# Optimization experiments

Hardware: AMD Instinct MI355X
Metric: run time of the kernel (lower is better)

Reference implementation:

```python
import jax, jax.numpy as jnp
import numpy as np
import math

EPS = 1e-5

def layernorm(x, w):
    mu = jnp.mean(x, axis=-1, keepdims=True)
    var = jnp.var(x, axis=-1, keepdims=True)
    return (x - mu) * jax.lax.rsqrt(var + EPS) * w

def setup_inputs() -> dict:
    key = jax.random.key(0)
    ks = jax.random.split(key, 6)
    B, T, C = 2, 2048, 768
    s = 0.02
    return {
        "x": jax.random.normal(ks[0], (B, T, C), jnp.float32),
        "w_ln1": jnp.ones((C,), jnp.float32),
        "w_attn": jax.random.normal(ks[1], (C, 3 * C), jnp.float32) * s,
        "w_attn_proj": jax.random.normal(ks[2], (C, C), jnp.float32) * s,
        "w_ln2": jnp.ones((C,), jnp.float32),
        "w_fc": jax.random.normal(ks[3], (C, 4 * C), jnp.float32) * s,
        "w_mlp_proj": jax.random.normal(ks[4], (4 * C, C), jnp.float32) * s,
    }

def _attention(x, w_attn, w_attn_proj, n_head):
    B, T, C = x.shape
    D = C // n_head
    qkv = x @ w_attn  # [B,T,3C]
    q, k, v = jnp.split(qkv, 3, axis=-1)
    # [B,H,T,D]
    q = q.reshape(B, T, n_head, D).transpose(0, 2, 1, 3)
    k = k.reshape(B, T, n_head, D).transpose(0, 2, 1, 3)
    v = v.reshape(B, T, n_head, D).transpose(0, 2, 1, 3)
    # squared L2 distance via ||q||^2 + ||k||^2 - 2 q.k (same math, no [B,H,T,T,D] tensor)
    q2 = jnp.sum(q * q, axis=-1)  # [B,H,T]
    k2 = jnp.sum(k * k, axis=-1)  # [B,H,T]
    qk = jnp.einsum('bhqd,bhkd->bhqk', q, k)
    sq_l2 = q2[..., :, None] + k2[..., None, :] - 2.0 * qk  # [B,H,T,T]
    scale = -1.0 / (2.0 * math.sqrt(D))
    scores = jnp.exp(sq_l2 * scale)
    causal = jnp.tril(jnp.ones((T, T), bool))
    scores = jnp.where(causal[None, None], scores, 0.0)
    y = jnp.einsum('bhqk,bhkd->bhqd', scores, v)
    y = y.transpose(0, 2, 1, 3).reshape(B, T, C)
    return y @ w_attn_proj

def reference(x, w_ln1, w_attn, w_attn_proj, w_ln2, w_fc, w_mlp_proj):
    n_head = 12
    x = x + _attention(layernorm(x, w_ln1), w_attn, w_attn_proj, n_head)
    h = layernorm(x, w_ln2)
    h = jax.nn.gelu(h @ w_fc, approximate=False) @ w_mlp_proj
    return x + h
```

## Files before the change

### kernel.cpp

```cpp
#include <hip/hip_runtime.h>

typedef unsigned short u16;
typedef unsigned int u32;
typedef short bf16x8 __attribute__((ext_vector_type(8)));
typedef float f32x4 __attribute__((ext_vector_type(4)));

#define AS1 __attribute__((address_space(1)))
#define AS3 __attribute__((address_space(3)))

__device__ __forceinline__ float bf2f(u16 u){ return __uint_as_float(((u32)u)<<16); }
__device__ __forceinline__ u16 f2bf(float f){
  u32 x = __float_as_uint(f);
  x += 0x7fffu + ((x>>16)&1u);
  return (u16)(x>>16);
}
__device__ __forceinline__ float gelu_exact(float x){
  return 0.5f*x*(1.f + erff(x*0.7071067811865475f));
}

__global__ __launch_bounds__(256) void transpose_cast(
    const float* __restrict__ w, u16* __restrict__ wt, int K, int N)
{
  __shared__ float t[32][33];
  int lx = threadIdx.x & 31, ly = threadIdx.x >> 5;
  int n0 = blockIdx.x*32, k0 = blockIdx.y*32;
  #pragma unroll
  for (int j=0;j<4;j++) t[ly+j*8][lx] = w[(long)(k0+ly+j*8)*N + n0+lx];
  __syncthreads();
  #pragma unroll
  for (int j=0;j<4;j++) wt[(long)(n0+ly+j*8)*K + k0+lx] = f2bf(t[lx][ly+j*8]);
}

__global__ __launch_bounds__(256) void ln_rows(
    const float* __restrict__ x, const float* __restrict__ w, u16* __restrict__ out)
{
  int row = blockIdx.x, tid = threadIdx.x;
  const float* xr = x + (long)row*768;
  float v0 = xr[tid], v1 = xr[tid+256], v2 = xr[tid+512];
  float s = v0+v1+v2, sq = v0*v0+v1*v1+v2*v2;
  #pragma unroll
  for (int o=32;o>=1;o>>=1){ s += __shfl_down(s,o); sq += __shfl_down(sq,o); }
  __shared__ float red[8];
  int wv = tid>>6, ln = tid&63;
  if (ln==0){ red[wv]=s; red[wv+4]=sq; }
  __syncthreads();
  float S  = red[0]+red[1]+red[2]+red[3];
  float SQ = red[4]+red[5]+red[6]+red[7];
  float mu = S*(1.f/768.f);
  float var = SQ*(1.f/768.f) - mu*mu;
  float rstd = rsqrtf(var + 1e-5f);
  u16* o = out + (long)row*768;
  o[tid]     = f2bf((v0-mu)*rstd*w[tid]);
  o[tid+256] = f2bf((v1-mu)*rstd*w[tid+256]);
  o[tid+512] = f2bf((v2-mu)*rstd*w[tid+512]);
}

__global__ __launch_bounds__(256) void v_transpose(
    const u16* __restrict__ qkv, u16* __restrict__ vt)
{
  __shared__ __align__(16) u16 t[64*72];
  int b = blockIdx.z, h = blockIdx.y, t0 = blockIdx.x*64;
  int tid = threadIdx.x;
  int r = tid>>2, g = tid&3, c8 = g*16;
  const u16* src = qkv + ((long)(b*2048 + t0 + r))*2304 + 1536 + h*64 + c8;
  int wcol = c8 ^ (((r>>4)&3)*16);
  *(uint4*)&t[r*72 + wcol]     = *(const uint4*)src;
  *(uint4*)&t[r*72 + wcol + 8] = *(const uint4*)(src + 8);
  __syncthreads();
  int d = r;
  int rcol = d ^ (g*16);
  u32 pk[8];
  #pragma unroll
  for (int j=0;j<8;j++){
    u32 lo = t[(c8+2*j  )*72 + rcol];
    u32 hi = t[(c8+2*j+1)*72 + rcol];
    pk[j] = lo | (hi<<16);
  }
  u16* dst = vt + ((long)((b*12+h)*64 + d))*2048 + t0 + c8;
  uint4 o0 = {pk[0],pk[1],pk[2],pk[3]};
  uint4 o1 = {pk[4],pk[5],pk[6],pk[7]};
  *(uint4*)dst       = o0;
  *(uint4*)(dst + 8) = o1;
}

template<int EPI>
__global__ __launch_bounds__(256) void gemm_bt(
    const u16* __restrict__ A, const u16* __restrict__ BT,
    int M, int N, int K,
    u16* __restrict__ outB,
    float* __restrict__ q2g, float* __restrict__ k2g)
{
  __shared__ __align__(16) u16 As[2][128*32];
  __shared__ __align__(16) u16 Bs[2][128*32];
  int tid = threadIdx.x;
  int gx = gridDim.x;
  int nwg = gx * gridDim.y;
  int flat = blockIdx.x + gx*blockIdx.y;
  int cpx = nwg >> 3;
  int swz = (flat & 7)*cpx + (flat >> 3);
  int n0 = (swz % gx)*128, m0 = (swz / gx)*128;
  int w = tid>>6, lane = tid&63, lr = lane&15, lg = lane>>4;
  int wr = w>>1, wc = w&1;
  f32x4 acc[4][4];
  f32x4 z = {0.f,0.f,0.f,0.f};
  #pragma unroll
  for (int m=0;m<4;m++)
    #pragma unroll
    for (int n=0;n<4;n++) acc[m][n] = z;
  int rr16 = lane>>2, cc = (lane&3)*8;
  const u16* gA0 = A  + (long)(m0 + (2*w  )*16 + rr16)*K + cc;
  const u16* gA1 = A  + (long)(m0 + (2*w+1)*16 + rr16)*K + cc;
  const u16* gB0 = BT + (long)(n0 + (2*w  )*16 + rr16)*K + cc;
  const u16* gB1 = BT + (long)(n0 + (2*w+1)*16 + rr16)*K + cc;
  int o0 = (2*w)*512, o1 = (2*w+1)*512;
  __builtin_amdgcn_global_load_lds((const AS1 void*)gA0, (AS3 void*)(&As[0][o0]), 16, 0, 0);
  __builtin_amdgcn_global_load_lds((const AS1 void*)gA1, (AS3 void*)(&As[0][o1]), 16, 0, 0);
  __builtin_amdgcn_global_load_lds((const AS1 void*)gB0, (AS3 void*)(&Bs[0][o0]), 16, 0, 0);
  __builtin_amdgcn_global_load_lds((const AS1 void*)gB1, (AS3 void*)(&Bs[0][o1]), 16, 0, 0);
  gA0 += 32; gA1 += 32; gB0 += 32; gB1 += 32;
  __syncthreads();
  int cur = 0;
  for (int k0=0; k0<K; k0+=32){
    if (k0+32 < K){
      int nx = cur^1;
      __builtin_amdgcn_global_load_lds((const AS1 void*)gA0, (AS3 void*)(&As[nx][o0]), 16, 0, 0);
      __builtin_amdgcn_global_load_lds((const AS1 void*)gA1, (AS3 void*)(&As[nx][o1]), 16, 0, 0);
      __builtin_amdgcn_global_load_lds((const AS1 void*)gB0, (AS3 void*)(&Bs[nx][o0]), 16, 0, 0);
      __builtin_amdgcn_global_load_lds((const AS1 void*)gB1, (AS3 void*)(&Bs[nx][o1]), 16, 0, 0);
      gA0 += 32; gA1 += 32; gB0 += 32; gB1 += 32;
    }
    const u16* Ac = As[cur];
    const u16* Bc = Bs[cur];
    bf16x8 af[4], bfr[4];
    #pragma unroll
    for (int m=0;m<4;m++) af[m]  = *(const bf16x8*)&Ac[(wr*64+m*16+lr)*32 + lg*8];
    #pragma unroll
    for (int n=0;n<4;n++) bfr[n] = *(const bf16x8*)&Bc[(wc*64+n*16+lr)*32 + lg*8];
    #pragma unroll
    for (int m=0;m<4;m++)
      #pragma unroll
      for (int n=0;n<4;n++)
        acc[m][n] = __builtin_amdgcn_mfma_f32_16x16x32_bf16(af[m], bfr[n], acc[m][n], 0,0,0);
    __syncthreads();
    cur ^= 1;
  }
  if (EPI==0){
    #pragma unroll
    for (int m=0;m<4;m++){
      float s2[4] = {0.f,0.f,0.f,0.f};
      #pragma unroll
      for (int n=0;n<4;n++)
        #pragma unroll
        for (int r=0;r<4;r++){
          int row = m0 + wr*64 + m*16 + lg*4 + r;
          int col = n0 + wc*64 + n*16 + lr;
          u16 ub = f2bf(acc[m][n][r]);
          outB[(long)row*N + col] = ub;
          float vr = bf2f(ub);
          s2[r] += vr*vr;
        }
      #pragma unroll
      for (int r=0;r<4;r++){
        float t = s2[r];
        t += __shfl_xor(t,1); t += __shfl_xor(t,2); t += __shfl_xor(t,4); t += __shfl_xor(t,8);
        if (lr==0){
          int head = (n0 + wc*64) >> 6;
          int row = m0 + wr*64 + m*16 + lg*4 + r;
          int bb = row >> 11, tt = row & 2047;
          if (head < 12)      q2g[((long)(bb*12 + head     ))*2048 + tt] = t;
          else if (head < 24) k2g[((long)(bb*12 + head - 12))*2048 + tt] = t;
        }
      }
    }
  } else {
    #pragma unroll
    for (int m=0;m<4;m++)
      #pragma unroll
      for (int n=0;n<4;n++)
        #pragma unroll
        for (int r=0;r<4;r++){
          int row = m0 + wr*64 + m*16 + lg*4 + r;
          int col = n0 + wc*64 + n*16 + lr;
          outB[(long)row*N + col] = f2bf(gelu_exact(acc[m][n][r]));
        }
  }
}

__global__ __launch_bounds__(256) void gemm_ks(
    const u16* __restrict__ A, const u16* __restrict__ BT,
    int M, int N, int K, int KS,
    float* __restrict__ pb)
{
  __shared__ __align__(16) u16 As[2][128*32];
  __shared__ __align__(16) u16 Bs[2][64*32];
  int tid = threadIdx.x;
  int n0 = blockIdx.x*64, m0 = blockIdx.y*128;
  int kbeg = blockIdx.z*KS;
  int w = tid>>6, lane = tid&63, lr = lane&15, lg = lane>>4;
  int wr = w>>1, wc = w&1;
  f32x4 acc[4][2];
  f32x4 z = {0.f,0.f,0.f,0.f};
  #pragma unroll
  for (int m=0;m<4;m++){ acc[m][0]=z; acc[m][1]=z; }
  int rr16 = lane>>2, cc = (lane&3)*8;
  const u16* gA0 = A  + (long)(m0 + (2*w  )*16 + rr16)*K + kbeg + cc;
  const u16* gA1 = A  + (long)(m0 + (2*w+1)*16 + rr16)*K + kbeg + cc;
  const u16* gB0 = BT + (long)(n0 + w*16 + rr16)*K + kbeg + cc;
  int oa0 = (2*w)*512, oa1 = (2*w+1)*512, ob = w*512;
  __builtin_amdgcn_global_load_lds((const AS1 void*)gA0, (AS3 void*)(&As[0][oa0]), 16, 0, 0);
  __builtin_amdgcn_global_load_lds((const AS1 void*)gA1, (AS3 void*)(&As[0][oa1]), 16, 0, 0);
  __builtin_amdgcn_global_load_lds((const AS1 void*)gB0, (AS3 void*)(&Bs[0][ob ]), 16, 0, 0);
  gA0 += 32; gA1 += 32; gB0 += 32;
  __syncthreads();
  int cur = 0;
  for (int k0=0; k0<KS; k0+=32){
    if (k0+32 < KS){
      int nx = cur^1;
      __builtin_amdgcn_global_load_lds((const AS1 void*)gA0, (AS3 void*)(&As[nx][oa0]), 16, 0, 0);
      __builtin_amdgcn_global_load_lds((const AS1 void*)gA1, (AS3 void*)(&As[nx][oa1]), 16, 0, 0);
      __builtin_amdgcn_global_load_lds((const AS1 void*)gB0, (AS3 void*)(&Bs[nx][ob ]), 16, 0, 0);
      gA0 += 32; gA1 += 32; gB0 += 32;
    }
    const u16* Ac = As[cur];
    const u16* Bc = Bs[cur];
    bf16x8 af[4], bfr[2];
    #pragma unroll
    for (int m=0;m<4;m++) af[m]  = *(const bf16x8*)&Ac[(wr*64+m*16+lr)*32 + lg*8];
    #pragma unroll
    for (int n=0;n<2;n++) bfr[n] = *(const bf16x8*)&Bc[(wc*32+n*16+lr)*32 + lg*8];
    #pragma unroll
    for (int m=0;m<4;m++)
      #pragma unroll
      for (int n=0;n<2;n++)
        acc[m][n] = __builtin_amdgcn_mfma_f32_16x16x32_bf16(af[m], bfr[n], acc[m][n], 0,0,0);
    __syncthreads();
    cur ^= 1;
  }
  long zofs = (long)blockIdx.z*M*N;
  #pragma unroll
  for (int m=0;m<4;m++)
    #pragma unroll
    for (int n=0;n<2;n++)
      #pragma unroll
      for (int r=0;r<4;r++){
        int row = m0 + wr*64 + m*16 + lg*4 + r;
        int col = n0 + wc*32 + n*16 + lr;
        pb[zofs + (long)row*N + col] = acc[m][n][r];
      }
}

__global__ __launch_bounds__(256) void reduce2(
    const float* __restrict__ p, const float* __restrict__ resid,
    float* __restrict__ out, long n)
{
  long i = ((long)blockIdx.x*256 + threadIdx.x)*4;
  f32x4 a = *(const f32x4*)(resid+i);
  f32x4 b = *(const f32x4*)(p+i);
  f32x4 c = *(const f32x4*)(p+n+i);
  *(f32x4*)(out+i) = a+b+c;
}

__global__ __launch_bounds__(128) void attn_fused(
    const u16* __restrict__ qkv, const u16* __restrict__ vt,
    const float* __restrict__ q2g, const float* __restrict__ k2g,
    u16* __restrict__ Y)
{
  constexpr int C3=2304, C=768, T=2048, PADP=72;
  __shared__ __align__(16) u16 Ks[2][4096];
  __shared__ __align__(16) u16 Vs[2][4096];
  __shared__ __align__(16) u16 Ps[2][16*PADP];
  int bz = blockIdx.x;
  int swzb = (bz&7)*96 + (bz>>3);
  int sp = swzb & 31;
  int hh = (swzb>>5) % 12;
  int b  = swzb / 384;
  int tid = threadIdx.x, w = tid>>6, lane = tid&63, lr = lane&15, lg = lane>>4;
  long base = (long)b*T;
  long bh = (long)(b*12 + hh);
  const u16* kbase = qkv + base*C3 + C + hh*64;
  const u16* vbase = vt + bh*64*(long)T;
  const float* k2p = k2g + bh*T;
  const float* q2p0 = q2g + bh*T;

  int rowl = lane>>3;
  int c16 = (lane&7) ^ rowl;
  const u16* kp[4]; const u16* vp[4];
  #pragma unroll
  for (int i=0;i<4;i++){
    int c = w*4 + i;
    kp[i] = kbase + (long)(c*8 + rowl)*C3 + c16*8;
    vp[i] = vbase + (long)(c*8 + rowl)*T + c16*8;
  }
  u16* Pw = &Ps[w][0];
  f32x4 z = {0.f,0.f,0.f,0.f};

  for (int ph=0; ph<2; ++ph){
    int s = ph ? 63 - sp : sp;
    int ktl = s>>1;
    int qg0 = s*32 + w*16;
    const u16* qrow = qkv + (base + qg0 + lr)*C3 + hh*64;
    bf16x8 aq0 = *(const bf16x8*)(qrow + lg*8);
    bf16x8 aq1 = *(const bf16x8*)(qrow + 32 + lg*8);
    float q2m[4]; int qg[4];
    #pragma unroll
    for (int rr=0;rr<4;rr++){
      qg[rr] = qg0 + lg*4 + rr;
      q2m[rr] = 0.0625f * q2p0[qg[rr]];
    }
    f32x4 accY[4];
    #pragma unroll
    for (int i=0;i<4;i++) accY[i] = z;

    #pragma unroll
    for (int i=0;i<4;i++){
      __builtin_amdgcn_global_load_lds((const AS1 void*)kp[i], (AS3 void*)&Ks[0][(w*4+i)*512], 16, 0, 0);
      __builtin_amdgcn_global_load_lds((const AS1 void*)vp[i], (AS3 void*)&Vs[0][(w*4+i)*512], 16, 0, 0);
    }
    float k2n[4];
    #pragma unroll
    for (int nf=0;nf<4;nf++) k2n[nf] = k2p[nf*16+lr];
    __syncthreads();

    int cur = 0;
    for (int kt=0; kt<=ktl; ++kt){
      float k2c[4];
      #pragma unroll
      for (int i=0;i<4;i++) k2c[i] = k2n[i];
      if (kt < ktl){
        long kadd = (long)(kt+1)*64*C3;
        long vadd = (long)(kt+1)*64;
        #pragma unroll
        for (int i=0;i<4;i++){
          __builtin_amdgcn_global_load_lds((const AS1 void*)(kp[i]+kadd), (AS3 void*)&Ks[cur^1][(w*4+i)*512], 16, 0, 0);
          __builtin_amdgcn_global_load_lds((const AS1 void*)(vp[i]+vadd), (AS3 void*)&Vs[cur^1][(w*4+i)*512], 16, 0, 0);
        }
        #pragma unroll
        for (int nf=0;nf<4;nf++) k2n[nf] = k2p[(kt+1)*64 + nf*16+lr];
      }
      const u16* Kc = &Ks[cur][0];
      const u16* Vc = &Vs[cur][0];
      int kg0 = kt*64;
      #pragma unroll
      for (int nf=0;nf<4;nf++){
        int row = nf*16 + lr;
        int sw0 = ((lg    ) ^ (row&7))*8;
        int sw1 = ((4 | lg) ^ (row&7))*8;
        f32x4 sc = z;
        sc = __builtin_amdgcn_mfma_f32_16x16x32_bf16(aq0, *(const bf16x8*)&Kc[row*64 + sw0], sc, 0,0,0);
        sc = __builtin_amdgcn_mfma_f32_16x16x32_bf16(aq1, *(const bf16x8*)&Kc[row*64 + sw1], sc, 0,0,0);
        int kg = kg0 + row;
        float k2m = 0.0625f * k2c[nf];
        #pragma unroll
        for (int rr=0;rr<4;rr++){
          float e = __expf(0.125f*sc[rr] - q2m[rr] - k2m);
          e = (kg <= qg[rr]) ? e : 0.f;
          Pw[(lg*4+rr)*PADP + row] = f2bf(e);
        }
      }
      __builtin_amdgcn_wave_barrier();
      asm volatile("s_waitcnt lgkmcnt(0)" ::: "memory");
      bf16x8 ap0 = *(const bf16x8*)&Pw[lr*PADP + lg*8];
      bf16x8 ap1 = *(const bf16x8*)&Pw[lr*PADP + 32 + lg*8];
      #pragma unroll
      for (int nf=0;nf<4;nf++){
        int row = nf*16 + lr;
        int sw0 = ((lg    ) ^ (row&7))*8;
        int sw1 = ((4 | lg) ^ (row&7))*8;
        accY[nf] = __builtin_amdgcn_mfma_f32_16x16x32_bf16(ap0, *(const bf16x8*)&Vc[row*64 + sw0], accY[nf], 0,0,0);
        accY[nf] = __builtin_amdgcn_mfma_f32_16x16x32_bf16(ap1, *(const bf16x8*)&Vc[row*64 + sw1], accY[nf], 0,0,0);
      }
      __syncthreads();
      cur ^= 1;
    }
    #pragma unroll
    for (int nf=0;nf<4;nf++)
      #pragma unroll
      for (int rr=0;rr<4;rr++)
        Y[(base + qg0 + lg*4 + rr)*C + hh*64 + nf*16 + lr] = f2bf(accY[nf][rr]);
  }
}

extern "C" void kernel_launch(void* const* d_in, const int* in_sizes, int n_in,
                              void* d_out, int out_size, void* d_ws, size_t ws_size,
                              hipStream_t stream)
{
  (void)in_sizes; (void)n_in; (void)out_size; (void)ws_size;
  const float* x      = (const float*)d_in[0];
  const float* w_ln1  = (const float*)d_in[1];
  const float* w_attn = (const float*)d_in[2];
  const float* w_ap   = (const float*)d_in[3];
  const float* w_ln2  = (const float*)d_in[4];
  const float* w_fc   = (const float*)d_in[5];
  const float* w_mlp  = (const float*)d_in[6];
  float* out = (float*)d_out;
  const int M = 4096, T = 2048;
  const long NROW = (long)M*768;

  u16* ws      = (u16*)d_ws;
  u16* wT_attn = ws;
  u16* wT_ap   = wT_attn + 2304*768;
  u16* wT_fc   = wT_ap   + 768*768;
  u16* wT_mlp  = wT_fc   + 3072*768;
  u16* xln     = wT_mlp  + 768*3072;
  u16* qkvb    = xln     + 4096*768;
  u16* Ybuf    = qkvb    + 4096*2304;
  u16* hbuf    = qkvb;
  float* x2    = (float*)(Ybuf + 4096*768);
  u16* vtb     = (u16*)(x2 + 4096*768);
  float* q2g   = (float*)(vtb + 2*12*64*2048);
  float* k2g   = q2g + 24*2048;
  float* pbuf  = k2g + 24*2048;

  dim3 blk(256);
  transpose_cast<<<dim3(2304/32,  768/32), blk, 0, stream>>>(w_attn, wT_attn,  768, 2304);
  transpose_cast<<<dim3( 768/32,  768/32), blk, 0, stream>>>(w_ap,   wT_ap,    768,  768);
  transpose_cast<<<dim3(3072/32,  768/32), blk, 0, stream>>>(w_fc,   wT_fc,    768, 3072);
  transpose_cast<<<dim3( 768/32, 3072/32), blk, 0, stream>>>(w_mlp,  wT_mlp,  3072,  768);

  ln_rows<<<dim3(M), blk, 0, stream>>>(x, w_ln1, xln);
  gemm_bt<0><<<dim3(2304/128, M/128), blk, 0, stream>>>(xln, wT_attn, M, 2304, 768, qkvb, q2g, k2g);
  v_transpose<<<dim3(T/64, 12, 2), blk, 0, stream>>>(qkvb, vtb);
  attn_fused<<<dim3(2*12*32), dim3(128), 0, stream>>>(qkvb, vtb, q2g, k2g, Ybuf);
  gemm_ks<<<dim3(768/64, M/128, 2), blk, 0, stream>>>(Ybuf, wT_ap, M, 768, 768, 384, pbuf);
  reduce2<<<dim3(NROW/1024), blk, 0, stream>>>(pbuf, x, x2, NROW);
  ln_rows<<<dim3(M), blk, 0, stream>>>(x2, w_ln2, xln);
  gemm_bt<1><<<dim3(3072/128, M/128), blk, 0, stream>>>(xln, wT_fc, M, 3072, 768, hbuf, nullptr, nullptr);
  gemm_ks<<<dim3(768/64, M/128, 2), blk, 0, stream>>>(hbuf, wT_mlp, M, 768, 3072, 1536, pbuf);
  reduce2<<<dim3(NROW/1024), blk, 0, stream>>>(pbuf, x2, out, NROW);
}
```

Measured before the change: 297.0 us.

## Fuse residual reduce with LayerNorm, single-barrier GEMM pipelines, exp2 attention softmax

Replaces the separate reduce2 and ln_rows launches with one reduce2_ln kernel that sums the split-K partials and the residual, then normalizes the row. This saves a launch and a round trip through x2. Both GEMM kernels now use one barrier per k-step with explicit vmcnt waits, so the next tile's loads overlap the MFMAs. The attention kernel swaps the MFMA operands so each lane owns one query row, folds the scale constants into exp2, loads k2 as vectors, and packs the P stores into 64-bit writes. The hand-written waitcnt counts depend on the exact number of outstanding loads, so they are fragile.

```diff
diff --git a/kernel.cpp b/kernel.cpp
--- a/kernel.cpp
+++ b/kernel.cpp
@@ -7,6 +7,12 @@
 
 #define AS1 __attribute__((address_space(1)))
 #define AS3 __attribute__((address_space(3)))
+
+#if __has_builtin(__builtin_amdgcn_exp2f)
+#define EX2(x) __builtin_amdgcn_exp2f(x)
+#else
+#define EX2(x) exp2f(x)
+#endif
 
 __device__ __forceinline__ float bf2f(u16 u){ return __uint_as_float(((u32)u)<<16); }
 __device__ __forceinline__ u16 f2bf(float f){
@@ -55,6 +61,36 @@
   o[tid+512] = f2bf((v2-mu)*rstd*w[tid+512]);
 }
 
+__global__ __launch_bounds__(256) void reduce2_ln(
+    const float* __restrict__ p, const float* __restrict__ resid,
+    const float* __restrict__ w, float* __restrict__ x2, u16* __restrict__ xln, long n)
+{
+  int row = blockIdx.x, tid = threadIdx.x;
+  long off = (long)row*768;
+  float v[3];
+  #pragma unroll
+  for (int j=0;j<3;j++){
+    long i = off + tid + j*256;
+    v[j] = resid[i] + p[i] + p[n+i];
+    x2[i] = v[j];
+  }
+  float s = v[0]+v[1]+v[2], sq = v[0]*v[0]+v[1]*v[1]+v[2]*v[2];
+  #pragma unroll
+  for (int o=32;o>=1;o>>=1){ s += __shfl_down(s,o); sq += __shfl_down(sq,o); }
+  __shared__ float red[8];
+  int wv = tid>>6, ln = tid&63;
+  if (ln==0){ red[wv]=s; red[wv+4]=sq; }
+  __syncthreads();
+  float S  = red[0]+red[1]+red[2]+red[3];
+  float SQ = red[4]+red[5]+red[6]+red[7];
+  float mu = S*(1.f/768.f);
+  float var = SQ*(1.f/768.f) - mu*mu;
+  float rstd = rsqrtf(var + 1e-5f);
+  #pragma unroll
+  for (int j=0;j<3;j++)
+    xln[off + tid + j*256] = f2bf((v[j]-mu)*rstd*w[tid + j*256]);
+}
+
 __global__ __launch_bounds__(256) void v_transpose(
     const u16* __restrict__ qkv, u16* __restrict__ vt)
 {
@@ -118,9 +154,9 @@
   __builtin_amdgcn_global_load_lds((const AS1 void*)gB0, (AS3 void*)(&Bs[0][o0]), 16, 0, 0);
   __builtin_amdgcn_global_load_lds((const AS1 void*)gB1, (AS3 void*)(&Bs[0][o1]), 16, 0, 0);
   gA0 += 32; gA1 += 32; gB0 += 32; gB1 += 32;
-  __syncthreads();
   int cur = 0;
   for (int k0=0; k0<K; k0+=32){
+    __builtin_amdgcn_s_barrier();
     if (k0+32 < K){
       int nx = cur^1;
       __builtin_amdgcn_global_load_lds((const AS1 void*)gA0, (AS3 void*)(&As[nx][o0]), 16, 0, 0);
@@ -128,7 +164,11 @@
       __builtin_amdgcn_global_load_lds((const AS1 void*)gB0, (AS3 void*)(&Bs[nx][o0]), 16, 0, 0);
       __builtin_amdgcn_global_load_lds((const AS1 void*)gB1, (AS3 void*)(&Bs[nx][o1]), 16, 0, 0);
       gA0 += 32; gA1 += 32; gB0 += 32; gB1 += 32;
-    }
+      asm volatile("s_waitcnt vmcnt(4)" ::: "memory");
+    } else {
+      asm volatile("s_waitcnt vmcnt(0)" ::: "memory");
+    }
+    __builtin_amdgcn_sched_barrier(0);
     const u16* Ac = As[cur];
     const u16* Bc = Bs[cur];
     bf16x8 af[4], bfr[4];
@@ -141,7 +181,6 @@
       #pragma unroll
       for (int n=0;n<4;n++)
         acc[m][n] = __builtin_amdgcn_mfma_f32_16x16x32_bf16(af[m], bfr[n], acc[m][n], 0,0,0);
-    __syncthreads();
     cur ^= 1;
   }
   if (EPI==0){
@@ -211,16 +250,20 @@
   __builtin_amdgcn_global_load_lds((const AS1 void*)gA1, (AS3 void*)(&As[0][oa1]), 16, 0, 0);
   __builtin_amdgcn_global_load_lds((const AS1 void*)gB0, (AS3 void*)(&Bs[0][ob ]), 16, 0, 0);
   gA0 += 32; gA1 += 32; gB0 += 32;
-  __syncthreads();
   int cur = 0;
   for (int k0=0; k0<KS; k0+=32){
+    __builtin_amdgcn_s_barrier();
     if (k0+32 < KS){
       int nx = cur^1;
       __builtin_amdgcn_global_load_lds((const AS1 void*)gA0, (AS3 void*)(&As[nx][oa0]), 16, 0, 0);
       __builtin_amdgcn_global_load_lds((const AS1 void*)gA1, (AS3 void*)(&As[nx][oa1]), 16, 0, 0);
       __builtin_amdgcn_global_load_lds((const AS1 void*)gB0, (AS3 void*)(&Bs[nx][ob ]), 16, 0, 0);
       gA0 += 32; gA1 += 32; gB0 += 32;
-    }
+      asm volatile("s_waitcnt vmcnt(3)" ::: "memory");
+    } else {
+      asm volatile("s_waitcnt vmcnt(0)" ::: "memory");
+    }
+    __builtin_amdgcn_sched_barrier(0);
     const u16* Ac = As[cur];
     const u16* Bc = Bs[cur];
     bf16x8 af[4], bfr[2];
@@ -233,7 +276,6 @@
       #pragma unroll
       for (int n=0;n<2;n++)
         acc[m][n] = __builtin_amdgcn_mfma_f32_16x16x32_bf16(af[m], bfr[n], acc[m][n], 0,0,0);
-    __syncthreads();
     cur ^= 1;
   }
   long zofs = (long)blockIdx.z*M*N;
@@ -266,6 +308,8 @@
     u16* __restrict__ Y)
 {
   constexpr int C3=2304, C=768, T=2048, PADP=72;
+  constexpr float C1 = 0.18033688f;
+  constexpr float S2 = 0.09016844f;
   __shared__ __align__(16) u16 Ks[2][4096];
   __shared__ __align__(16) u16 Vs[2][4096];
   __shared__ __align__(16) u16 Ps[2][16*PADP];
@@ -301,12 +345,8 @@
     const u16* qrow = qkv + (base + qg0 + lr)*C3 + hh*64;
     bf16x8 aq0 = *(const bf16x8*)(qrow + lg*8);
     bf16x8 aq1 = *(const bf16x8*)(qrow + 32 + lg*8);
-    float q2m[4]; int qg[4];
-    #pragma unroll
-    for (int rr=0;rr<4;rr++){
-      qg[rr] = qg0 + lg*4 + rr;
-      q2m[rr] = 0.0625f * q2p0[qg[rr]];
-    }
+    const float q2v = S2 * q2p0[qg0 + lr];
+    const int qg_s = qg0 + lr;
     f32x4 accY[4];
     #pragma unroll
     for (int i=0;i<4;i++) accY[i] = z;
@@ -316,16 +356,19 @@
       __builtin_amdgcn_global_load_lds((const AS1 void*)kp[i], (AS3 void*)&Ks[0][(w*4+i)*512], 16, 0, 0);
       __builtin_amdgcn_global_load_lds((const AS1 void*)vp[i], (AS3 void*)&Vs[0][(w*4+i)*512], 16, 0, 0);
     }
-    float k2n[4];
-    #pragma unroll
-    for (int nf=0;nf<4;nf++) k2n[nf] = k2p[nf*16+lr];
+    f32x4 k2n4[4];
+    #pragma unroll
+    for (int nf=0;nf<4;nf++){
+      f32x4 t4 = *(const f32x4*)&k2p[nf*16 + lg*4];
+      k2n4[nf] = t4 * S2;
+    }
     __syncthreads();
 
     int cur = 0;
     for (int kt=0; kt<=ktl; ++kt){
-      float k2c[4];
-      #pragma unroll
-      for (int i=0;i<4;i++) k2c[i] = k2n[i];
+      f32x4 k2c4[4];
+      #pragma unroll
+      for (int i=0;i<4;i++) k2c4[i] = k2n4[i];
       if (kt < ktl){
         long kadd = (long)(kt+1)*64*C3;
         long vadd = (long)(kt+1)*64;
@@ -335,7 +378,10 @@
           __builtin_amdgcn_global_load_lds((const AS1 void*)(vp[i]+vadd), (AS3 void*)&Vs[cur^1][(w*4+i)*512], 16, 0, 0);
         }
         #pragma unroll
-        for (int nf=0;nf<4;nf++) k2n[nf] = k2p[(kt+1)*64 + nf*16+lr];
+        for (int nf=0;nf<4;nf++){
+          f32x4 t4 = *(const f32x4*)&k2p[(kt+1)*64 + nf*16 + lg*4];
+          k2n4[nf] = t4 * S2;
+        }
       }
       const u16* Kc = &Ks[cur][0];
       const u16* Vc = &Vs[cur][0];
@@ -345,17 +391,24 @@
         int row = nf*16 + lr;
         int sw0 = ((lg    ) ^ (row&7))*8;
         int sw1 = ((4 | lg) ^ (row&7))*8;
+        bf16x8 kb0 = *(const bf16x8*)&Kc[row*64 + sw0];
+        bf16x8 kb1 = *(const bf16x8*)&Kc[row*64 + sw1];
         f32x4 sc = z;
-        sc = __builtin_amdgcn_mfma_f32_16x16x32_bf16(aq0, *(const bf16x8*)&Kc[row*64 + sw0], sc, 0,0,0);
-        sc = __builtin_amdgcn_mfma_f32_16x16x32_bf16(aq1, *(const bf16x8*)&Kc[row*64 + sw1], sc, 0,0,0);
-        int kg = kg0 + row;
-        float k2m = 0.0625f * k2c[nf];
+        sc = __builtin_amdgcn_mfma_f32_16x16x32_bf16(kb0, aq0, sc, 0,0,0);
+        sc = __builtin_amdgcn_mfma_f32_16x16x32_bf16(kb1, aq1, sc, 0,0,0);
+        int kb = kg0 + nf*16 + lg*4;
+        u16 pbk[4];
         #pragma unroll
         for (int rr=0;rr<4;rr++){
-          float e = __expf(0.125f*sc[rr] - q2m[rr] - k2m);
-          e = (kg <= qg[rr]) ? e : 0.f;
-          Pw[(lg*4+rr)*PADP + row] = f2bf(e);
-        }
+          float arg = sc[rr]*C1 - q2v - k2c4[nf][rr];
+          float e = EX2(arg);
+          e = (kb + rr <= qg_s) ? e : 0.f;
+          pbk[rr] = f2bf(e);
+        }
+        uint2 pk2;
+        pk2.x = (u32)pbk[0] | ((u32)pbk[1]<<16);
+        pk2.y = (u32)pbk[2] | ((u32)pbk[3]<<16);
+        *(uint2*)&Pw[lr*PADP + nf*16 + lg*4] = pk2;
       }
       __builtin_amdgcn_wave_barrier();
       asm volatile("s_waitcnt lgkmcnt(0)" ::: "memory");
@@ -422,8 +475,7 @@
   v_transpose<<<dim3(T/64, 12, 2), blk, 0, stream>>>(qkvb, vtb);
   attn_fused<<<dim3(2*12*32), dim3(128), 0, stream>>>(qkvb, vtb, q2g, k2g, Ybuf);
   gemm_ks<<<dim3(768/64, M/128, 2), blk, 0, stream>>>(Ybuf, wT_ap, M, 768, 768, 384, pbuf);
-  reduce2<<<dim3(NROW/1024), blk, 0, stream>>>(pbuf, x, x2, NROW);
-  ln_rows<<<dim3(M), blk, 0, stream>>>(x2, w_ln2, xln);
+  reduce2_ln<<<dim3(M), blk, 0, stream>>>(pbuf, x, w_ln2, x2, xln, NROW);
   gemm_bt<1><<<dim3(3072/128, M/128), blk, 0, stream>>>(xln, wT_fc, M, 3072, 768, hbuf, nullptr, nullptr);
   gemm_ks<<<dim3(768/64, M/128, 2), blk, 0, stream>>>(hbuf, wT_mlp, M, 768, 3072, 1536, pbuf);
   reduce2<<<dim3(NROW/1024), blk, 0, stream>>>(pbuf, x2, out, NROW);
```

New measurement: 291.5 us. No clear change (-1.8%).
